# Optimization experiments

Hardware: AMD Instinct MI355X
Metric: run time of the kernel (lower is better)

Reference implementation:

```python
import jax, jax.numpy as jnp
import numpy as np

VOCAB = 32000
EMB = 32
HID = 64
B = 1024
T = 512


def setup_inputs() -> dict:
    key = jax.random.key(0)
    ks = jax.random.split(key, 8)
    s_e = 1.0 / np.sqrt(EMB)
    s_h = 1.0 / np.sqrt(HID)
    return {
        "x": jax.random.randint(ks[0], (B, T), 0, VOCAB),
        "emb": jax.random.normal(ks[1], (VOCAB, EMB), jnp.float32),
        "W_ih": jax.random.uniform(ks[2], (4 * HID, EMB), jnp.float32, -s_h, s_h),
        "W_hh": jax.random.uniform(ks[3], (4 * HID, HID), jnp.float32, -s_h, s_h),
        "b_ih": jax.random.uniform(ks[4], (4 * HID,), jnp.float32, -s_h, s_h),
        "b_hh": jax.random.uniform(ks[5], (4 * HID,), jnp.float32, -s_h, s_h),
        "fc_W": jax.random.uniform(ks[6], (VOCAB, HID), jnp.float32, -s_h, s_h),
        "fc_b": jax.random.uniform(ks[7], (VOCAB,), jnp.float32, -s_h, s_h),
    }


def reference(x, emb, W_ih, W_hh, b_ih, b_hh, fc_W, fc_b):
    e = emb[x]  # [B, T, EMB]
    # Precompute input contribution to all gates for all timesteps: [B, T, 4H]
    xg = jnp.einsum("bte,ge->btg", e, W_ih) + b_ih + b_hh
    xg_t = jnp.transpose(xg, (1, 0, 2))  # [T, B, 4H] for scan over time

    def step(carry, xg_step):
        h, c = carry
        gates = xg_step + h @ W_hh.T  # [B, 4H]
        i, f, g, o = jnp.split(gates, 4, axis=-1)  # torch gate order i,f,g,o
        i = jax.nn.sigmoid(i)
        f = jax.nn.sigmoid(f)
        g = jnp.tanh(g)
        o = jax.nn.sigmoid(o)
        c = f * c + i * g
        h = o * jnp.tanh(c)
        return (h, c), None

    h0 = jnp.zeros((x.shape[0], HID), e.dtype)
    c0 = jnp.zeros((x.shape[0], HID), e.dtype)
    (h_last, _), _ = jax.lax.scan(step, (h0, c0), xg_t)
    # out[:, -1, :] of the LSTM is just the final hidden state
    return h_last @ fc_W.T + fc_b  # [B, VOCAB]
```

## Files before the change

### kernel.cpp

```cpp
#include <hip/hip_runtime.h>
#include <cstddef>
#include <cstdint>

#define VOCAB 32000
#define EMB 32
#define HID 64
#define NG 256
#define BATCH 1024
#define SEQ 512
#define NB 4
#define ROWB 72

typedef short short8 __attribute__((ext_vector_type(8)));
typedef _Float16 half8 __attribute__((ext_vector_type(8)));
typedef float floatx4 __attribute__((ext_vector_type(4)));
typedef int int4v __attribute__((ext_vector_type(4)));

union FragH {
  half8 h;
  int4v v;
};

__device__ __forceinline__ float fast_sig(float x) {
  return __builtin_amdgcn_rcpf(1.0f + __expf(-x));
}
__device__ __forceinline__ float fast_tanh(float x) {
  return fmaf(-2.0f, __builtin_amdgcn_rcpf(__expf(2.0f * x) + 1.0f), 1.0f);
}

#define K1_ROWS 32
__global__ __launch_bounds__(256) void build_table(
    const float* __restrict__ emb, const float* __restrict__ W_ih,
    const float* __restrict__ b_ih, const float* __restrict__ b_hh,
    float* __restrict__ table) {
  __shared__ __align__(16) float erow[K1_ROWS * EMB];
  const int tid = threadIdx.x;
  const int v0 = blockIdx.x * K1_ROWS;

  float w[EMB];
#pragma unroll
  for (int e = 0; e < EMB; e += 4) {
    const float4 t = *(const float4*)&W_ih[tid * EMB + e];
    w[e] = t.x; w[e + 1] = t.y; w[e + 2] = t.z; w[e + 3] = t.w;
  }
  const float bsum = b_ih[tid] + b_hh[tid];

  ((float4*)erow)[tid] = ((const float4*)&emb[(size_t)v0 * EMB])[tid];
  __syncthreads();

#pragma unroll 4
  for (int r = 0; r < K1_ROWS; ++r) {
    float acc = bsum;
#pragma unroll
    for (int e = 0; e < EMB; ++e) acc += erow[r * EMB + e] * w[e];
    table[(size_t)(v0 + r) * NG + tid] = acc;
  }
}

__global__ __launch_bounds__(256) void lstm_mfma(
    const int* __restrict__ x, const float* __restrict__ table,
    const float* __restrict__ W_hh, float* __restrict__ h_out) {
  __shared__ __align__(16) _Float16 Hs[2][16 * ROWB];
  __shared__ int xls[NB * SEQ];

  const int tid = threadIdx.x;
  const int w = tid >> 6;
  const int lane = tid & 63;
  const int quad = lane >> 4;
  const int col = lane & 15;
  const int blk = blockIdx.x;
  const int myhid = w * 16 + col;

  {
    int* hz = (int*)&Hs[0][0];
    const int nz = (int)(sizeof(Hs) / 4);
    for (int i = tid; i < nz; i += 256) hz[i] = 0;
  }
  {
    const int* xsrc = &x[(size_t)blk * NB * SEQ];
    for (int i = tid; i < NB * SEQ; i += 256) xls[i] = xsrc[i];
  }

  FragH Bf[4][2];
#pragma unroll
  for (int ti = 0; ti < 4; ++ti) {
    const int n = (w + ti * 4) * 16 + col;
#pragma unroll
    for (int ko = 0; ko < 2; ++ko) {
      const float* src = &W_hh[n * HID + ko * 32 + quad * 8];
#pragma unroll
      for (int j = 0; j < 8; ++j) Bf[ti][ko].h[j] = (_Float16)src[j];
    }
  }

  floatx4 acc[4];
#pragma unroll
  for (int ti = 0; ti < 4; ++ti) acc[ti] = (floatx4){0.f, 0.f, 0.f, 0.f};

  float c = 0.0f, hcur = 0.0f;

  __syncthreads();

  const int xrow = quad * SEQ;
  const float* __restrict__ tb = table + myhid;

  float xgA[4], xgB[4];
  {
    const float* bp = tb + ((size_t)(unsigned)xls[xrow + 0] << 8);
#pragma unroll
    for (int ti = 0; ti < 4; ++ti) xgA[ti] = bp[ti * 64];
    const float* bq = tb + ((size_t)(unsigned)xls[xrow + 1] << 8);
#pragma unroll
    for (int ti = 0; ti < 4; ++ti) xgB[ti] = bq[ti * 64];
  }

  auto step = [&](float (&XG)[4], const int RB, const int TT) {
    const int abase = col * ROWB + quad * 8;
    FragH A0, A1;
    A0.v = *(const int4v*)&Hs[RB][abase];
    A1.v = *(const int4v*)&Hs[RB][abase + 32];

#pragma unroll
    for (int ti = 0; ti < 4; ++ti) {
      floatx4 a = acc[ti];
      a[0] = XG[ti];
      a = __builtin_amdgcn_mfma_f32_16x16x32_f16(A0.h, Bf[ti][0].h, a, 0, 0, 0);
      a = __builtin_amdgcn_mfma_f32_16x16x32_f16(A1.h, Bf[ti][1].h, a, 0, 0, 0);
      acc[ti] = a;
    }

    {
      const int tn = (TT + 2 < SEQ) ? TT + 2 : SEQ - 1;
      const float* bp = tb + ((size_t)(unsigned)xls[xrow + tn] << 8);
#pragma unroll
      for (int ti = 0; ti < 4; ++ti) XG[ti] = bp[ti * 64];
    }

    {
      const float gi = fast_sig(acc[0][0]);
      const float gf = fast_sig(acc[1][0]);
      const float gg = fast_tanh(acc[2][0]);
      const float go = fast_sig(acc[3][0]);
      c = gf * c + gi * gg;
      hcur = go * fast_tanh(c);
      Hs[RB ^ 1][(quad * 4) * ROWB + myhid] = (_Float16)hcur;
    }
    __syncthreads();
  };

  for (int t = 0; t < SEQ; t += 2) {
    step(xgA, 0, t);
    step(xgB, 1, t + 1);
  }

  h_out[((size_t)blk * NB + quad) * HID + myhid] = hcur;
}

#define FC_BB 128
#define FC_BV 128
#define FC_PAD 4
__global__ __launch_bounds__(256) void fc_kernel(
    const float* __restrict__ h, const float* __restrict__ fc_W,
    const float* __restrict__ fc_b, float* __restrict__ out) {
  __shared__ __align__(16) float sh[HID][FC_BB + FC_PAD];
  __shared__ __align__(16) float sw[HID][FC_BV + FC_PAD];
  const int tid = threadIdx.x;
  const int v0 = blockIdx.x * FC_BV;
  const int b0 = blockIdx.y * FC_BB;
  const int ti = tid >> 4;
  const int tj = tid & 15;

  const float4 bias0 = *(const float4*)&fc_b[v0 + tj * 4];
  const float4 bias1 = *(const float4*)&fc_b[v0 + 64 + tj * 4];

  {
    const float4* src = (const float4*)&h[(size_t)b0 * HID];
#pragma unroll
    for (int i = 0; i < 8; ++i) {
      const int idx = tid + i * 256;
      const float4 t = src[idx];
      const int bl = idx >> 4;
      const int k = (idx * 4) & (HID - 1);
      sh[k][bl] = t.x; sh[k + 1][bl] = t.y; sh[k + 2][bl] = t.z; sh[k + 3][bl] = t.w;
    }
    const float4* wsrc = (const float4*)&fc_W[(size_t)v0 * HID];
#pragma unroll
    for (int i = 0; i < 8; ++i) {
      const int idx = tid + i * 256;
      const float4 t = wsrc[idx];
      const int vl = idx >> 4;
      const int k = (idx * 4) & (HID - 1);
      sw[k][vl] = t.x; sw[k + 1][vl] = t.y; sw[k + 2][vl] = t.z; sw[k + 3][vl] = t.w;
    }
  }
  __syncthreads();

  float acc[8][8];
#pragma unroll
  for (int i = 0; i < 8; ++i)
#pragma unroll
    for (int j = 0; j < 8; ++j) acc[i][j] = 0.0f;

#pragma unroll 4
  for (int k = 0; k < HID; ++k) {
    const float4 h0 = *(const float4*)&sh[k][ti * 8];
    const float4 h1 = *(const float4*)&sh[k][ti * 8 + 4];
    const float4 w0 = *(const float4*)&sw[k][tj * 4];
    const float4 w1 = *(const float4*)&sw[k][64 + tj * 4];
    const float hv[8] = {h0.x, h0.y, h0.z, h0.w, h1.x, h1.y, h1.z, h1.w};
    const float wv[8] = {w0.x, w0.y, w0.z, w0.w, w1.x, w1.y, w1.z, w1.w};
#pragma unroll
    for (int i = 0; i < 8; ++i)
#pragma unroll
      for (int j = 0; j < 8; ++j) acc[i][j] += hv[i] * wv[j];
  }

#pragma unroll
  for (int i = 0; i < 8; ++i) {
    const size_t row = (size_t)(b0 + ti * 8 + i) * VOCAB;
    float4 o0, o1;
    o0.x = acc[i][0] + bias0.x; o0.y = acc[i][1] + bias0.y;
    o0.z = acc[i][2] + bias0.z; o0.w = acc[i][3] + bias0.w;
    o1.x = acc[i][4] + bias1.x; o1.y = acc[i][5] + bias1.y;
    o1.z = acc[i][6] + bias1.z; o1.w = acc[i][7] + bias1.w;
    *(float4*)&out[row + v0 + tj * 4] = o0;
    *(float4*)&out[row + v0 + 64 + tj * 4] = o1;
  }
}

extern "C" void kernel_launch(void* const* d_in, const int* in_sizes, int n_in,
                              void* d_out, int out_size, void* d_ws, size_t ws_size,
                              hipStream_t stream) {
  const int* x = (const int*)d_in[0];
  const float* emb = (const float*)d_in[1];
  const float* W_ih = (const float*)d_in[2];
  const float* W_hh = (const float*)d_in[3];
  const float* b_ih = (const float*)d_in[4];
  const float* b_hh = (const float*)d_in[5];
  const float* fc_W = (const float*)d_in[6];
  const float* fc_b = (const float*)d_in[7];
  float* out = (float*)d_out;

  float* table = out;
  float* hbuf = (float*)d_ws;

  build_table<<<VOCAB / K1_ROWS, 256, 0, stream>>>(emb, W_ih, b_ih, b_hh, table);
  lstm_mfma<<<BATCH / NB, 256, 0, stream>>>(x, table, W_hh, hbuf);
  dim3 g3(VOCAB / FC_BV, BATCH / FC_BB);
  fc_kernel<<<g3, 256, 0, stream>>>(hbuf, fc_W, fc_b, out);
}
```

Measured before the change: 361.6 us.

## Interleave gate table per hidden unit and deepen gather prefetch to eight steps

The precomputed input-gate table is now written with the four gates of each hidden unit stored next to each other. The recurrent kernel can then fetch all four gate inputs for a timestep with a single float4 load instead of four strided scalar loads. The prefetch distance grows from two to eight timesteps using eight rotating registers, which hides the latency of the dependent gather behind more steps. The gate input is added after the MFMA rather than injected into the accumulator, at the cost of more live registers.

```diff
diff --git a/kernel.cpp b/kernel.cpp
--- a/kernel.cpp
+++ b/kernel.cpp
@@ -10,6 +10,7 @@
 #define SEQ 512
 #define NB 4
 #define ROWB 72
+#define PFD 8
 
 typedef short short8 __attribute__((ext_vector_type(8)));
 typedef _Float16 half8 __attribute__((ext_vector_type(8)));
@@ -36,14 +37,15 @@
   __shared__ __align__(16) float erow[K1_ROWS * EMB];
   const int tid = threadIdx.x;
   const int v0 = blockIdx.x * K1_ROWS;
+  const int gidx = (tid & 3) * 64 + (tid >> 2);
 
   float w[EMB];
 #pragma unroll
   for (int e = 0; e < EMB; e += 4) {
-    const float4 t = *(const float4*)&W_ih[tid * EMB + e];
+    const float4 t = *(const float4*)&W_ih[gidx * EMB + e];
     w[e] = t.x; w[e + 1] = t.y; w[e + 2] = t.z; w[e + 3] = t.w;
   }
-  const float bsum = b_ih[tid] + b_hh[tid];
+  const float bsum = b_ih[gidx] + b_hh[gidx];
 
   ((float4*)erow)[tid] = ((const float4*)&emb[(size_t)v0 * EMB])[tid];
   __syncthreads();
@@ -93,54 +95,46 @@
     }
   }
 
-  floatx4 acc[4];
-#pragma unroll
-  for (int ti = 0; ti < 4; ++ti) acc[ti] = (floatx4){0.f, 0.f, 0.f, 0.f};
-
   float c = 0.0f, hcur = 0.0f;
 
   __syncthreads();
 
   const int xrow = quad * SEQ;
-  const float* __restrict__ tb = table + myhid;
-
-  float xgA[4], xgB[4];
-  {
-    const float* bp = tb + ((size_t)(unsigned)xls[xrow + 0] << 8);
-#pragma unroll
-    for (int ti = 0; ti < 4; ++ti) xgA[ti] = bp[ti * 64];
-    const float* bq = tb + ((size_t)(unsigned)xls[xrow + 1] << 8);
-#pragma unroll
-    for (int ti = 0; ti < 4; ++ti) xgB[ti] = bq[ti * 64];
-  }
-
-  auto step = [&](float (&XG)[4], const int RB, const int TT) {
+  const float* __restrict__ tb4 = table + (size_t)myhid * 4;
+
+  auto gather = [&](int tt) -> float4 {
+    return *(const float4*)(tb4 + ((size_t)(unsigned)xls[xrow + tt] << 8));
+  };
+
+  float4 xg0 = gather(0), xg1 = gather(1), xg2 = gather(2), xg3 = gather(3);
+  float4 xg4 = gather(4), xg5 = gather(5), xg6 = gather(6), xg7 = gather(7);
+
+  auto step = [&](float4& XG, const int RB, const int TT) {
+    const float xi = XG.x, xf = XG.y, xgg = XG.z, xo = XG.w;
+    {
+      const int tn = (TT + PFD < SEQ) ? TT + PFD : SEQ - 1;
+      XG = gather(tn);
+    }
+
     const int abase = col * ROWB + quad * 8;
     FragH A0, A1;
     A0.v = *(const int4v*)&Hs[RB][abase];
     A1.v = *(const int4v*)&Hs[RB][abase + 32];
 
+    floatx4 g4[4];
 #pragma unroll
     for (int ti = 0; ti < 4; ++ti) {
-      floatx4 a = acc[ti];
-      a[0] = XG[ti];
+      floatx4 a = (floatx4){0.f, 0.f, 0.f, 0.f};
       a = __builtin_amdgcn_mfma_f32_16x16x32_f16(A0.h, Bf[ti][0].h, a, 0, 0, 0);
       a = __builtin_amdgcn_mfma_f32_16x16x32_f16(A1.h, Bf[ti][1].h, a, 0, 0, 0);
-      acc[ti] = a;
+      g4[ti] = a;
     }
 
     {
-      const int tn = (TT + 2 < SEQ) ? TT + 2 : SEQ - 1;
-      const float* bp = tb + ((size_t)(unsigned)xls[xrow + tn] << 8);
-#pragma unroll
-      for (int ti = 0; ti < 4; ++ti) XG[ti] = bp[ti * 64];
-    }
-
-    {
-      const float gi = fast_sig(acc[0][0]);
-      const float gf = fast_sig(acc[1][0]);
-      const float gg = fast_tanh(acc[2][0]);
-      const float go = fast_sig(acc[3][0]);
+      const float gi = fast_sig(g4[0][0] + xi);
+      const float gf = fast_sig(g4[1][0] + xf);
+      const float gg = fast_tanh(g4[2][0] + xgg);
+      const float go = fast_sig(g4[3][0] + xo);
       c = gf * c + gi * gg;
       hcur = go * fast_tanh(c);
       Hs[RB ^ 1][(quad * 4) * ROWB + myhid] = (_Float16)hcur;
@@ -148,9 +142,15 @@
     __syncthreads();
   };
 
-  for (int t = 0; t < SEQ; t += 2) {
-    step(xgA, 0, t);
-    step(xgB, 1, t + 1);
+  for (int t = 0; t < SEQ; t += 8) {
+    step(xg0, 0, t);
+    step(xg1, 1, t + 1);
+    step(xg2, 0, t + 2);
+    step(xg3, 1, t + 3);
+    step(xg4, 0, t + 4);
+    step(xg5, 1, t + 5);
+    step(xg6, 0, t + 6);
+    step(xg7, 1, t + 7);
   }
 
   h_out[((size_t)blk * NB + quad) * HID + myhid] = hcur;
```

New measurement: 337.5 us. 1.07x faster.
